# Kernel optimization log

Measured on AMD Instinct MI355X. Metric: run time of the kernel, lower is better.

## Reference

```python
import jax, jax.numpy as jnp
import numpy as np

B, T, D, H, F = 8, 1024, 512, 8, 2048
DK = D // H
EPS = 1e-3  # Keras LayerNormalization default epsilon
NEG = -1e9


def layer_norm(x, g, b):
    mu = jnp.mean(x, axis=-1, keepdims=True)
    var = jnp.mean(jnp.square(x - mu), axis=-1, keepdims=True)
    return (x - mu) * jax.lax.rsqrt(var + EPS) * g + b


def setup_inputs() -> dict:
    key = jax.random.key(0)
    ks = jax.random.split(key, 16)
    s = 1.0 / np.sqrt(D)
    sf = 1.0 / np.sqrt(F)
    x = jax.random.normal(ks[0], (B, T, D), dtype=jnp.float32)
    # binary attention mask (1 = attend). Random block-sparse-ish pattern.
    mask = (jax.random.uniform(ks[1], (B, 1, T, T)) > 0.15).astype(jnp.float32)
    return {
        "x": x,
        "mask": mask,
        "ln_in_g": jnp.ones((D,), jnp.float32),
        "ln_in_b": jnp.zeros((D,), jnp.float32),
        "Wq": jax.random.normal(ks[2], (D, D), jnp.float32) * s,
        "bq": jnp.zeros((D,), jnp.float32),
        "Wk": jax.random.normal(ks[3], (D, D), jnp.float32) * s,
        "bk": jnp.zeros((D,), jnp.float32),
        "Wv": jax.random.normal(ks[4], (D, D), jnp.float32) * s,
        "bv": jnp.zeros((D,), jnp.float32),
        "ln1_g": jnp.ones((D,), jnp.float32),
        "ln1_b": jnp.zeros((D,), jnp.float32),
        "W1": jax.random.normal(ks[5], (D, F), jnp.float32) * s,
        "b1": jnp.zeros((F,), jnp.float32),
        "W2": jax.random.normal(ks[6], (F, D), jnp.float32) * sf,
        "b2": jnp.zeros((D,), jnp.float32),
        "ln2_g": jnp.ones((D,), jnp.float32),
        "ln2_b": jnp.zeros((D,), jnp.float32),
    }


def reference(x, mask, ln_in_g, ln_in_b, Wq, bq, Wk, bk, Wv, bv,
              ln1_g, ln1_b, W1, b1, W2, b2, ln2_g, ln2_b):
    bs = x.shape[0]
    h = layer_norm(x, ln_in_g, ln_in_b)                      # [B,T,D]
    # QKV projections, split heads -> [B,H,T,DK]
    q = (h @ Wq + bq).reshape(bs, -1, H, DK).transpose(0, 2, 1, 3)
    k = (h @ Wk + bk).reshape(bs, -1, H, DK).transpose(0, 2, 1, 3)
    v = (h @ Wv + bv).reshape(bs, -1, H, DK).transpose(0, 2, 1, 3)
    scores = jnp.einsum('bhtd,bhsd->bhts', q, k) / np.sqrt(DK)
    scores = scores + NEG * (1.0 - mask)                     # additive mask
    probs = jax.nn.softmax(scores, axis=-1)                  # dropout: identity at inference
    attn = jnp.einsum('bhts,bhsd->bhtd', probs, v)
    attn = attn.transpose(0, 2, 1, 3).reshape(bs, -1, H * DK)
    # residual with ORIGINAL inputs (pre-ln_in), as in call() -> attend(inputs,...)
    attn = attn + x
    a = layer_norm(attn, ln1_g, ln1_b)
    f = jax.nn.relu(a @ W1 + b1) @ W2 + b2
    out = layer_norm(f + a, ln2_g, ln2_b)
    return out
```

## Files before the change

### kernel.cpp

```cpp
#include <hip/hip_runtime.h>

typedef unsigned short u16;
typedef unsigned long long u64;
typedef __bf16 bf16x8 __attribute__((ext_vector_type(8)));
typedef float f32x4 __attribute__((ext_vector_type(4)));

#define B_ 8
#define T_ 1024
#define D_ 512
#define H_ 8
#define DK_ 64
#define F_ 2048

__device__ __forceinline__ u16 f2bf(float f) {
    unsigned u = __float_as_uint(f);
    u += 0x7fffu + ((u >> 16) & 1u);
    return (u16)(u >> 16);
}

__device__ __forceinline__ void tile_transcvt(
    const float* __restrict__ W, u16* __restrict__ WT, int K, int N, int k0, int n0,
    u16 (*t)[72])
{
    const int tid = threadIdx.x;
    const int r = tid >> 2, c4 = (tid & 3) * 16;
    const float* src = W + (size_t)(k0 + r) * N + n0 + c4;
#pragma unroll
    for (int j = 0; j < 16; j += 4) {
        float4 v = *(const float4*)(src + j);
        t[r][c4 + j]     = f2bf(v.x);
        t[r][c4 + j + 1] = f2bf(v.y);
        t[r][c4 + j + 2] = f2bf(v.z);
        t[r][c4 + j + 3] = f2bf(v.w);
    }
    __syncthreads();
    u16 tmp[16];
#pragma unroll
    for (int j = 0; j < 16; ++j) tmp[j] = t[c4 + j][r];
    u16* dst = WT + (size_t)(n0 + r) * K + k0 + c4;
    *(uint4*)dst       = *(uint4*)&tmp[0];
    *(uint4*)(dst + 8) = *(uint4*)&tmp[8];
}

__global__ __launch_bounds__(256) void prep_all(
    const float* __restrict__ Wq, const float* __restrict__ Wk, const float* __restrict__ Wv,
    const float* __restrict__ bq, const float* __restrict__ bk, const float* __restrict__ bv,
    const float* __restrict__ W1, const float* __restrict__ W2,
    const float* __restrict__ mask,
    u16* __restrict__ WqkvT, u16* __restrict__ W1T, u16* __restrict__ W2T,
    float* __restrict__ bias, u64* __restrict__ Mb)
{
    __shared__ u16 t[64][72];
    const int blk = blockIdx.x;
    const int tid = threadIdx.x;
    if (blk < 192) {
        const int k0 = (blk & 7) * 64;
        const int n0 = (blk >> 3) * 64;
        const float* W = (n0 < 512) ? Wq : (n0 < 1024 ? Wk : Wv);
        if (k0 == 0 && tid < 64) {
            int n = n0 + tid;
            bias[n] = (n < 512) ? bq[n] : (n < 1024 ? bk[n - 512] : bv[n - 1024]);
        }
        const int r = tid >> 2, c4 = (tid & 3) * 16;
        const float* src = W + (size_t)(k0 + r) * 512 + (n0 & 511) + c4;
#pragma unroll
        for (int j = 0; j < 16; j += 4) {
            float4 v = *(const float4*)(src + j);
            t[r][c4 + j]     = f2bf(v.x);
            t[r][c4 + j + 1] = f2bf(v.y);
            t[r][c4 + j + 2] = f2bf(v.z);
            t[r][c4 + j + 3] = f2bf(v.w);
        }
        __syncthreads();
        u16 tmp[16];
#pragma unroll
        for (int j = 0; j < 16; ++j) tmp[j] = t[c4 + j][r];
        u16* dst = WqkvT + (size_t)(n0 + r) * 512 + k0 + c4;
        *(uint4*)dst       = *(uint4*)&tmp[0];
        *(uint4*)(dst + 8) = *(uint4*)&tmp[8];
    } else if (blk < 448) {
        const int idx = blk - 192;
        tile_transcvt(W1, W1T, 512, 2048, (idx & 7) * 64, (idx >> 3) * 64, t);
    } else if (blk < 704) {
        const int idx = blk - 448;
        tile_transcvt(W2, W2T, 2048, 512, (idx & 31) * 64, (idx >> 5) * 64, t);
    } else {
        const int idx = blk - 704;
        int gw = (idx * 256 + tid) >> 6;
        int lane = tid & 63;
#pragma unroll
        for (int i = 0; i < 16; ++i) {
            size_t chunk = (size_t)gw * 16 + i;
            float v = mask[chunk * 64 + lane];
            u64 bm = __ballot(v > 0.5f);
            if (lane == 0) Mb[chunk] = bm;
        }
    }
}

__global__ __launch_bounds__(256) void ln_kernel(
    const float* __restrict__ X, const float* __restrict__ R,
    const float* __restrict__ g, const float* __restrict__ bt,
    u16* __restrict__ ob, float* __restrict__ of)
{
    int wave = threadIdx.x >> 6, lane = threadIdx.x & 63;
    int row = blockIdx.x * 4 + wave;
    size_t base = (size_t)row * D_ + lane * 8;
    float v[8];
    float4 a0 = *(const float4*)(X + base);
    float4 a1 = *(const float4*)(X + base + 4);
    v[0]=a0.x; v[1]=a0.y; v[2]=a0.z; v[3]=a0.w;
    v[4]=a1.x; v[5]=a1.y; v[6]=a1.z; v[7]=a1.w;
    if (R) {
        float4 r0 = *(const float4*)(R + base);
        float4 r1 = *(const float4*)(R + base + 4);
        v[0]+=r0.x; v[1]+=r0.y; v[2]+=r0.z; v[3]+=r0.w;
        v[4]+=r1.x; v[5]+=r1.y; v[6]+=r1.z; v[7]+=r1.w;
    }
    float s = 0.f, q = 0.f;
#pragma unroll
    for (int j = 0; j < 8; ++j) { s += v[j]; q += v[j] * v[j]; }
#pragma unroll
    for (int off = 32; off > 0; off >>= 1) {
        s += __shfl_xor(s, off);
        q += __shfl_xor(q, off);
    }
    float mu = s * (1.0f / D_);
    float var = q * (1.0f / D_) - mu * mu;
    float rstd = rsqrtf(var + 1e-3f);
    int c0 = lane * 8;
    float y[8];
#pragma unroll
    for (int j = 0; j < 8; ++j) y[j] = (v[j] - mu) * rstd * g[c0 + j] + bt[c0 + j];
    if (ob) {
        u16 t[8];
#pragma unroll
        for (int j = 0; j < 8; ++j) t[j] = f2bf(y[j]);
        *(uint4*)(ob + base) = *(uint4*)t;
    }
    if (of) {
        float4 o0, o1;
        o0.x=y[0]; o0.y=y[1]; o0.z=y[2]; o0.w=y[3];
        o1.x=y[4]; o1.y=y[5]; o1.z=y[6]; o1.w=y[7];
        *(float4*)(of + base) = o0;
        *(float4*)(of + base + 4) = o1;
    }
}

template<int BN, int RELU, int OUTBF>
__global__ __launch_bounds__(256) void gemm_db(
    const u16* __restrict__ A, const u16* __restrict__ BT,
    const float* __restrict__ bias, u16* __restrict__ Cb,
    float* __restrict__ Cf, int M, int N, int K)
{
    constexpr int NI = BN / 32;
    __shared__ u16 As[2][128 * 32];
    __shared__ u16 Bs[2][BN * 32];
    const int nb = gridDim.x;
    const int flat = blockIdx.y * nb + blockIdx.x;
    const int xcd = flat & 7;
    const int idx = flat >> 3;
    const int nblk = idx >> 3;
    const int mblk = xcd * 8 + (idx & 7);
    const int tid = threadIdx.x;
    const int wave = tid >> 6, lane = tid & 63;
    const int quad = lane >> 4, l16 = lane & 15;
    const int wr = wave >> 1, wc = wave & 1;
    const int rowBase = mblk * 128;
    const int colBase = nblk * BN;
    const int lr = lane >> 2;
    const int lc = (lane & 3) * 8;
    const u16* Abase = A  + (size_t)(rowBase + lr) * K + lc;
    const u16* Bbase = BT + (size_t)(colBase + lr) * K + lc;

    auto stage = [&](int k0, int buf) {
#pragma unroll
        for (int c = 0; c < 2; ++c) {
            int chunk = wave * 2 + c;
            const u16* gp = Abase + (size_t)(chunk * 16) * K + k0;
            __builtin_amdgcn_global_load_lds(
                (const __attribute__((address_space(1))) unsigned int*)gp,
                (__attribute__((address_space(3))) unsigned int*)&As[buf][chunk * 512],
                16, 0, 0);
        }
#pragma unroll
        for (int c = 0; c < BN / 64; ++c) {
            int chunk = wave * (BN / 64) + c;
            const u16* gp = Bbase + (size_t)(chunk * 16) * K + k0;
            __builtin_amdgcn_global_load_lds(
                (const __attribute__((address_space(1))) unsigned int*)gp,
                (__attribute__((address_space(3))) unsigned int*)&Bs[buf][chunk * 512],
                16, 0, 0);
        }
    };

    f32x4 acc[4][NI] = {};
    stage(0, 0);
    for (int k0 = 0; k0 < K; k0 += 32) {
        const int buf = (k0 >> 5) & 1;
        __syncthreads();
        if (k0 + 32 < K) stage(k0 + 32, buf ^ 1);
        bf16x8 af[4], bfr[NI];
#pragma unroll
        for (int i = 0; i < 4; ++i)
            af[i] = *(const bf16x8*)&As[buf][(wr * 64 + i * 16 + l16) * 32 + quad * 8];
#pragma unroll
        for (int j = 0; j < NI; ++j)
            bfr[j] = *(const bf16x8*)&Bs[buf][(wc * (BN / 2) + j * 16 + l16) * 32 + quad * 8];
#pragma unroll
        for (int i = 0; i < 4; ++i)
#pragma unroll
            for (int j = 0; j < NI; ++j)
                acc[i][j] = __builtin_amdgcn_mfma_f32_16x16x32_bf16(af[i], bfr[j], acc[i][j], 0, 0, 0);
    }
#pragma unroll
    for (int i = 0; i < 4; ++i) {
        int row0 = rowBase + wr * 64 + i * 16 + quad * 4;
#pragma unroll
        for (int j = 0; j < NI; ++j) {
            int col = colBase + wc * (BN / 2) + j * 16 + l16;
            float bv = bias[col];
#pragma unroll
            for (int r = 0; r < 4; ++r) {
                float v = acc[i][j][r] + bv;
                if (RELU) v = fmaxf(v, 0.0f);
                if (OUTBF) Cb[(size_t)(row0 + r) * N + col] = f2bf(v);
                else       Cf[(size_t)(row0 + r) * N + col] = v;
            }
        }
    }
}

__global__ __launch_bounds__(256) void vtrans(const u16* __restrict__ QKV, u16* __restrict__ Vt)
{
    int blk = blockIdx.x;
    int bh = blk >> 4;
    int t0 = (blk & 15) * 64;
    int b = bh >> 3, h = bh & 7;
    __shared__ u16 tile[64][72];
    int tid = threadIdx.x;
    int r = tid >> 2;
    int c = (tid & 3) * 16;
    const u16* src = QKV + ((size_t)(b * T_) + t0 + r) * (3 * D_) + 2 * D_ + h * DK_ + c;
    *(uint4*)&tile[r][c]     = *(const uint4*)(src);
    *(uint4*)&tile[r][c + 8] = *(const uint4*)(src + 8);
    __syncthreads();
    u16 tmp[16];
#pragma unroll
    for (int j = 0; j < 16; ++j) tmp[j] = tile[c + j][r];
    u16* dst = Vt + ((size_t)bh * DK_ + r) * T_ + t0 + c;
    *(uint4*)dst       = *(uint4*)&tmp[0];
    *(uint4*)(dst + 8) = *(uint4*)&tmp[8];
}

#define APAD 72
__global__ __launch_bounds__(256) void attn_kernel(
    const u16* __restrict__ QKV, const u16* __restrict__ Vt,
    const u64* __restrict__ Mb, float* __restrict__ Out)
{
    const int flat = blockIdx.x + 16 * (blockIdx.y + 8 * blockIdx.z);
    const int xcd = flat & 7, slot = flat >> 3;
    const int bh = xcd * 8 + (slot >> 4);
    const int qt = slot & 15;
    const int b = bh >> 3, h = bh & 7;
    const int qBase = qt * 64;
    const int tid = threadIdx.x;
    const int wave = tid >> 6, lane = tid & 63;
    const int quad = lane >> 4, l16 = lane & 15;
    __shared__ u16 Ks[64][APAD];
    __shared__ u16 Vs[64][APAD];
    __shared__ u16 Ps[4][16][APAD];

    const int qRow = qBase + wave * 16 + l16;
    const u16* qptr = QKV + ((size_t)(b * T_) + qRow) * (3 * D_) + h * DK_;
    bf16x8 qf0 = *(const bf16x8*)(qptr + quad * 8);
    bf16x8 qf1 = *(const bf16x8*)(qptr + 32 + quad * 8);

    float l_i[4] = {0.f, 0.f, 0.f, 0.f};
    f32x4 o[4] = {{0,0,0,0},{0,0,0,0},{0,0,0,0},{0,0,0,0}};

    const int sr = tid >> 2;
    const int sc = (tid & 3) * 8;
    const u16* Kg = QKV + (size_t)(b * T_) * (3 * D_) + D_ + h * DK_;
    const u16* Vg = Vt + (size_t)(b * H_ + h) * DK_ * T_;
    const u64* Mg = Mb + ((size_t)(b * T_) + qBase + wave * 16 + quad * 4) * (T_ / 64);

    uint4 kb0 = *(const uint4*)(Kg + (size_t)sr * (3 * D_) + sc);
    uint4 kb1 = *(const uint4*)(Kg + (size_t)sr * (3 * D_) + sc + 32);
    uint4 vb0 = *(const uint4*)(Vg + (size_t)sr * T_ + sc);
    uint4 vb1 = *(const uint4*)(Vg + (size_t)sr * T_ + sc + 32);
    u64 m64[4];
#pragma unroll
    for (int r = 0; r < 4; ++r) m64[r] = Mg[(size_t)r * (T_ / 64)];

    for (int s0 = 0; s0 < T_; s0 += 64) {
        __syncthreads();
        *(uint4*)&Ks[sr][sc]      = kb0;
        *(uint4*)&Ks[sr][sc + 32] = kb1;
        *(uint4*)&Vs[sr][sc]      = vb0;
        *(uint4*)&Vs[sr][sc + 32] = vb1;
        __syncthreads();
        u64 mcur[4];
#pragma unroll
        for (int r = 0; r < 4; ++r) mcur[r] = m64[r];
        if (s0 + 64 < T_) {
            int s1 = s0 + 64;
            kb0 = *(const uint4*)(Kg + (size_t)(s1 + sr) * (3 * D_) + sc);
            kb1 = *(const uint4*)(Kg + (size_t)(s1 + sr) * (3 * D_) + sc + 32);
            vb0 = *(const uint4*)(Vg + (size_t)sr * T_ + s1 + sc);
            vb1 = *(const uint4*)(Vg + (size_t)sr * T_ + s1 + sc + 32);
#pragma unroll
            for (int r = 0; r < 4; ++r) m64[r] = Mg[(size_t)r * (T_ / 64) + (s1 >> 6)];
        }

#pragma unroll
        for (int n = 0; n < 4; ++n) {
            f32x4 s4 = {0.f, 0.f, 0.f, 0.f};
            bf16x8 kf0 = *(const bf16x8*)&Ks[n * 16 + l16][quad * 8];
            bf16x8 kf1 = *(const bf16x8*)&Ks[n * 16 + l16][32 + quad * 8];
            s4 = __builtin_amdgcn_mfma_f32_16x16x32_bf16(qf0, kf0, s4, 0, 0, 0);
            s4 = __builtin_amdgcn_mfma_f32_16x16x32_bf16(qf1, kf1, s4, 0, 0, 0);
#pragma unroll
            for (int r = 0; r < 4; ++r) {
                float p = __expf(fmaf(s4[r], 0.125f, -10.0f));
                p = ((mcur[r] >> (n * 16 + l16)) & 1ull) ? p : 0.0f;
                l_i[r] += p;
                Ps[wave][quad * 4 + r][n * 16 + l16] = f2bf(p);
            }
        }
        bf16x8 pf0 = *(const bf16x8*)&Ps[wave][l16][quad * 8];
        bf16x8 pf1 = *(const bf16x8*)&Ps[wave][l16][32 + quad * 8];
#pragma unroll
        for (int dt = 0; dt < 4; ++dt) {
            bf16x8 vf0 = *(const bf16x8*)&Vs[dt * 16 + l16][quad * 8];
            bf16x8 vf1 = *(const bf16x8*)&Vs[dt * 16 + l16][32 + quad * 8];
            o[dt] = __builtin_amdgcn_mfma_f32_16x16x32_bf16(pf0, vf0, o[dt], 0, 0, 0);
            o[dt] = __builtin_amdgcn_mfma_f32_16x16x32_bf16(pf1, vf1, o[dt], 0, 0, 0);
        }
    }
#pragma unroll
    for (int off = 1; off < 16; off <<= 1) {
#pragma unroll
        for (int r = 0; r < 4; ++r) l_i[r] += __shfl_xor(l_i[r], off);
    }
    float inv[4];
#pragma unroll
    for (int r = 0; r < 4; ++r) inv[r] = 1.0f / l_i[r];
    const int orow = qBase + wave * 16 + quad * 4;
    float* Ob = Out + ((size_t)(b * T_) + orow) * D_ + h * DK_;
#pragma unroll
    for (int dt = 0; dt < 4; ++dt) {
#pragma unroll
        for (int r = 0; r < 4; ++r)
            Ob[(size_t)r * D_ + dt * 16 + l16] = o[dt][r] * inv[r];
    }
}

extern "C" void kernel_launch(void* const* d_in, const int* in_sizes, int n_in,
                              void* d_out, int out_size, void* d_ws, size_t ws_size,
                              hipStream_t stream)
{
    const float* x       = (const float*)d_in[0];
    const float* mask    = (const float*)d_in[1];
    const float* ln_in_g = (const float*)d_in[2];
    const float* ln_in_b = (const float*)d_in[3];
    const float* Wq      = (const float*)d_in[4];
    const float* bq      = (const float*)d_in[5];
    const float* Wk      = (const float*)d_in[6];
    const float* bk      = (const float*)d_in[7];
    const float* Wv      = (const float*)d_in[8];
    const float* bv      = (const float*)d_in[9];
    const float* ln1_g   = (const float*)d_in[10];
    const float* ln1_b   = (const float*)d_in[11];
    const float* W1      = (const float*)d_in[12];
    const float* b1      = (const float*)d_in[13];
    const float* W2      = (const float*)d_in[14];
    const float* b2      = (const float*)d_in[15];
    const float* ln2_g   = (const float*)d_in[16];
    const float* ln2_b   = (const float*)d_in[17];
    float* out = (float*)d_out;

    char* ws = (char*)d_ws;
    size_t off = 0;
    auto alloc = [&](size_t bytes) -> void* {
        void* p = ws + off;
        off = (off + bytes + 255) & ~(size_t)255;
        return p;
    };
    u16*   WqkvT   = (u16*)alloc((size_t)1536 * 512 * 2);
    u16*   W1T     = (u16*)alloc((size_t)2048 * 512 * 2);
    u16*   W2T     = (u16*)alloc((size_t)512 * 2048 * 2);
    float* bias_q  = (float*)alloc(1536 * 4);
    u64*   Mb      = (u64*)alloc((size_t)B_ * T_ * (T_ / 64) * 8);
    u16*   h_bf    = (u16*)alloc((size_t)8192 * 512 * 2);
    u16*   QKV     = (u16*)alloc((size_t)8192 * 1536 * 2);
    u16*   Vt      = (u16*)alloc((size_t)B_ * H_ * DK_ * T_ * 2);
    float* attn    = (float*)alloc((size_t)8192 * 512 * 4);
    u16*   a_bf    = (u16*)alloc((size_t)8192 * 512 * 2);
    float* a_f     = (float*)alloc((size_t)8192 * 512 * 4);
    u16*   f1      = (u16*)alloc((size_t)8192 * 2048 * 2);
    float* f2      = (float*)alloc((size_t)8192 * 512 * 4);
    if (off > ws_size) return;

    prep_all<<<2752, 256, 0, stream>>>(Wq, Wk, Wv, bq, bk, bv, W1, W2, mask,
                                       WqkvT, W1T, W2T, bias_q, Mb);

    ln_kernel<<<2048, 256, 0, stream>>>(x, nullptr, ln_in_g, ln_in_b, h_bf, nullptr);

    gemm_db<128, 0, 1><<<dim3(1536 / 128, 8192 / 128), 256, 0, stream>>>(
        h_bf, WqkvT, bias_q, QKV, nullptr, 8192, 1536, 512);

    vtrans<<<1024, 256, 0, stream>>>(QKV, Vt);

    attn_kernel<<<dim3(T_ / 64, H_, B_), 256, 0, stream>>>(QKV, Vt, Mb, attn);

    ln_kernel<<<2048, 256, 0, stream>>>(attn, x, ln1_g, ln1_b, a_bf, a_f);

    gemm_db<128, 1, 1><<<dim3(2048 / 128, 8192 / 128), 256, 0, stream>>>(
        a_bf, W1T, b1, f1, nullptr, 8192, 2048, 512);

    gemm_db<64, 0, 0><<<dim3(512 / 64, 8192 / 128), 256, 0, stream>>>(
        f1, W2T, b2, nullptr, f2, 8192, 512, 2048);

    ln_kernel<<<2048, 256, 0, stream>>>(f2, a_f, ln2_g, ln2_b, nullptr, out);
}
```

Before: 291.8 us.

## Split-K FFN2 with atomics, bf16 attention output, and bias-prefilled accumulator

The FFN2 GEMM is split into two K halves accumulated with float atomicAdd into f2, which the LN1 kernel prefills with b2. This doubles the block count for the 512-wide GEMM. Attention now writes bf16 instead of fp32, and the fp32 copy of the LN1 output is dropped, so the final LN reads the bf16 residual. Mask-word loads in attention are no longer prefetched a tile ahead. The changes cut memory traffic and raise parallelism, at the cost of some precision and atomic contention.

Result: no change. 296.9 us (+1.7%).

```diff
diff --git a/kernel.cpp b/kernel.cpp
--- a/kernel.cpp
+++ b/kernel.cpp
@@ -16,6 +16,9 @@
     unsigned u = __float_as_uint(f);
     u += 0x7fffu + ((u >> 16) & 1u);
     return (u16)(u >> 16);
+}
+__device__ __forceinline__ float bf2f(u16 v) {
+    return __uint_as_float((unsigned)v << 16);
 }
 
 __device__ __forceinline__ void tile_transcvt(
@@ -98,24 +101,51 @@
     }
 }
 
-__global__ __launch_bounds__(256) void ln_kernel(
-    const float* __restrict__ X, const float* __restrict__ R,
+template<int XBF, int RBF, int OB, int OF, int FILL>
+__global__ __launch_bounds__(256) void ln_t(
+    const void* __restrict__ Xv, const void* __restrict__ Rv,
     const float* __restrict__ g, const float* __restrict__ bt,
-    u16* __restrict__ ob, float* __restrict__ of)
+    u16* __restrict__ ob, float* __restrict__ of,
+    const float* __restrict__ fillsrc, float* __restrict__ filldst)
 {
     int wave = threadIdx.x >> 6, lane = threadIdx.x & 63;
     int row = blockIdx.x * 4 + wave;
     size_t base = (size_t)row * D_ + lane * 8;
+    int c0 = lane * 8;
     float v[8];
-    float4 a0 = *(const float4*)(X + base);
-    float4 a1 = *(const float4*)(X + base + 4);
-    v[0]=a0.x; v[1]=a0.y; v[2]=a0.z; v[3]=a0.w;
-    v[4]=a1.x; v[5]=a1.y; v[6]=a1.z; v[7]=a1.w;
-    if (R) {
-        float4 r0 = *(const float4*)(R + base);
-        float4 r1 = *(const float4*)(R + base + 4);
-        v[0]+=r0.x; v[1]+=r0.y; v[2]+=r0.z; v[3]+=r0.w;
-        v[4]+=r1.x; v[5]+=r1.y; v[6]+=r1.z; v[7]+=r1.w;
+    if (XBF) {
+        const u16* X = (const u16*)Xv;
+        uint4 a = *(const uint4*)(X + base);
+        u16 tu[8]; *(uint4*)tu = a;
+#pragma unroll
+        for (int j = 0; j < 8; ++j) v[j] = bf2f(tu[j]);
+    } else {
+        const float* X = (const float*)Xv;
+        float4 a0 = *(const float4*)(X + base);
+        float4 a1 = *(const float4*)(X + base + 4);
+        v[0]=a0.x; v[1]=a0.y; v[2]=a0.z; v[3]=a0.w;
+        v[4]=a1.x; v[5]=a1.y; v[6]=a1.z; v[7]=a1.w;
+    }
+    if (Rv) {
+        if (RBF) {
+            const u16* R = (const u16*)Rv;
+            uint4 a = *(const uint4*)(R + base);
+            u16 tu[8]; *(uint4*)tu = a;
+#pragma unroll
+            for (int j = 0; j < 8; ++j) v[j] += bf2f(tu[j]);
+        } else {
+            const float* R = (const float*)Rv;
+            float4 r0 = *(const float4*)(R + base);
+            float4 r1 = *(const float4*)(R + base + 4);
+            v[0]+=r0.x; v[1]+=r0.y; v[2]+=r0.z; v[3]+=r0.w;
+            v[4]+=r1.x; v[5]+=r1.y; v[6]+=r1.z; v[7]+=r1.w;
+        }
+    }
+    if (FILL) {
+        float4 f0 = *(const float4*)(fillsrc + c0);
+        float4 f1v = *(const float4*)(fillsrc + c0 + 4);
+        *(float4*)(filldst + base) = f0;
+        *(float4*)(filldst + base + 4) = f1v;
     }
     float s = 0.f, q = 0.f;
 #pragma unroll
@@ -128,17 +158,16 @@
     float mu = s * (1.0f / D_);
     float var = q * (1.0f / D_) - mu * mu;
     float rstd = rsqrtf(var + 1e-3f);
-    int c0 = lane * 8;
     float y[8];
 #pragma unroll
     for (int j = 0; j < 8; ++j) y[j] = (v[j] - mu) * rstd * g[c0 + j] + bt[c0 + j];
-    if (ob) {
+    if (OB) {
         u16 t[8];
 #pragma unroll
         for (int j = 0; j < 8; ++j) t[j] = f2bf(y[j]);
         *(uint4*)(ob + base) = *(uint4*)t;
     }
-    if (of) {
+    if (OF) {
         float4 o0, o1;
         o0.x=y[0]; o0.y=y[1]; o0.z=y[2]; o0.w=y[3];
         o1.x=y[4]; o1.y=y[5]; o1.z=y[6]; o1.w=y[7];
@@ -147,11 +176,11 @@
     }
 }
 
-template<int BN, int RELU, int OUTBF>
+template<int BN, int RELU, int OUT>
 __global__ __launch_bounds__(256) void gemm_db(
     const u16* __restrict__ A, const u16* __restrict__ BT,
     const float* __restrict__ bias, u16* __restrict__ Cb,
-    float* __restrict__ Cf, int M, int N, int K)
+    float* __restrict__ Cf, int N, int K, int KS)
 {
     constexpr int NI = BN / 32;
     __shared__ u16 As[2][128 * 32];
@@ -170,8 +199,9 @@
     const int colBase = nblk * BN;
     const int lr = lane >> 2;
     const int lc = (lane & 3) * 8;
-    const u16* Abase = A  + (size_t)(rowBase + lr) * K + lc;
-    const u16* Bbase = BT + (size_t)(colBase + lr) * K + lc;
+    const int kOff = blockIdx.z * KS;
+    const u16* Abase = A  + (size_t)(rowBase + lr) * K + kOff + lc;
+    const u16* Bbase = BT + (size_t)(colBase + lr) * K + kOff + lc;
 
     auto stage = [&](int k0, int buf) {
 #pragma unroll
@@ -196,10 +226,10 @@
 
     f32x4 acc[4][NI] = {};
     stage(0, 0);
-    for (int k0 = 0; k0 < K; k0 += 32) {
+    for (int k0 = 0; k0 < KS; k0 += 32) {
         const int buf = (k0 >> 5) & 1;
         __syncthreads();
-        if (k0 + 32 < K) stage(k0 + 32, buf ^ 1);
+        if (k0 + 32 < KS) stage(k0 + 32, buf ^ 1);
         bf16x8 af[4], bfr[NI];
 #pragma unroll
         for (int i = 0; i < 4; ++i)
@@ -219,13 +249,14 @@
 #pragma unroll
         for (int j = 0; j < NI; ++j) {
             int col = colBase + wc * (BN / 2) + j * 16 + l16;
-            float bv = bias[col];
+            float bv = (OUT == 2) ? 0.0f : bias[col];
 #pragma unroll
             for (int r = 0; r < 4; ++r) {
                 float v = acc[i][j][r] + bv;
                 if (RELU) v = fmaxf(v, 0.0f);
-                if (OUTBF) Cb[(size_t)(row0 + r) * N + col] = f2bf(v);
-                else       Cf[(size_t)(row0 + r) * N + col] = v;
+                if (OUT == 2)      atomicAdd(&Cf[(size_t)(row0 + r) * N + col], v);
+                else if (OUT == 1) Cb[(size_t)(row0 + r) * N + col] = f2bf(v);
+                else               Cf[(size_t)(row0 + r) * N + col] = v;
             }
         }
     }
@@ -256,7 +287,7 @@
 #define APAD 72
 __global__ __launch_bounds__(256) void attn_kernel(
     const u16* __restrict__ QKV, const u16* __restrict__ Vt,
-    const u64* __restrict__ Mb, float* __restrict__ Out)
+    const u64* __restrict__ Mb, u16* __restrict__ Out)
 {
     const int flat = blockIdx.x + 16 * (blockIdx.y + 8 * blockIdx.z);
     const int xcd = flat & 7, slot = flat >> 3;
@@ -289,9 +320,6 @@
     uint4 kb1 = *(const uint4*)(Kg + (size_t)sr * (3 * D_) + sc + 32);
     uint4 vb0 = *(const uint4*)(Vg + (size_t)sr * T_ + sc);
     uint4 vb1 = *(const uint4*)(Vg + (size_t)sr * T_ + sc + 32);
-    u64 m64[4];
-#pragma unroll
-    for (int r = 0; r < 4; ++r) m64[r] = Mg[(size_t)r * (T_ / 64)];
 
     for (int s0 = 0; s0 < T_; s0 += 64) {
         __syncthreads();
@@ -300,18 +328,17 @@
         *(uint4*)&Vs[sr][sc]      = vb0;
         *(uint4*)&Vs[sr][sc + 32] = vb1;
         __syncthreads();
-        u64 mcur[4];
-#pragma unroll
-        for (int r = 0; r < 4; ++r) mcur[r] = m64[r];
         if (s0 + 64 < T_) {
             int s1 = s0 + 64;
             kb0 = *(const uint4*)(Kg + (size_t)(s1 + sr) * (3 * D_) + sc);
             kb1 = *(const uint4*)(Kg + (size_t)(s1 + sr) * (3 * D_) + sc + 32);
             vb0 = *(const uint4*)(Vg + (size_t)sr * T_ + s1 + sc);
             vb1 = *(const uint4*)(Vg + (size_t)sr * T_ + s1 + sc + 32);
-#pragma unroll
-            for (int r = 0; r < 4; ++r) m64[r] = Mg[(size_t)r * (T_ / 64) + (s1 >> 6)];
-        }
+        }
+
+        u64 m64[4];
+#pragma unroll
+        for (int r = 0; r < 4; ++r) m64[r] = Mg[(size_t)r * (T_ / 64) + (s0 >> 6)];
 
 #pragma unroll
         for (int n = 0; n < 4; ++n) {
@@ -323,7 +350,7 @@
 #pragma unroll
             for (int r = 0; r < 4; ++r) {
                 float p = __expf(fmaf(s4[r], 0.125f, -10.0f));
-                p = ((mcur[r] >> (n * 16 + l16)) & 1ull) ? p : 0.0f;
+                p = ((m64[r] >> (n * 16 + l16)) & 1ull) ? p : 0.0f;
                 l_i[r] += p;
                 Ps[wave][quad * 4 + r][n * 16 + l16] = f2bf(p);
             }
@@ -347,12 +374,12 @@
 #pragma unroll
     for (int r = 0; r < 4; ++r) inv[r] = 1.0f / l_i[r];
     const int orow = qBase + wave * 16 + quad * 4;
-    float* Ob = Out + ((size_t)(b * T_) + orow) * D_ + h * DK_;
+    u16* Ob = Out + ((size_t)(b * T_) + orow) * D_ + h * DK_;
 #pragma unroll
     for (int dt = 0; dt < 4; ++dt) {
 #pragma unroll
         for (int r = 0; r < 4; ++r)
-            Ob[(size_t)r * D_ + dt * 16 + l16] = o[dt][r] * inv[r];
+            Ob[(size_t)r * D_ + dt * 16 + l16] = f2bf(o[dt][r] * inv[r]);
     }
 }
 
@@ -395,9 +422,8 @@
     u16*   h_bf    = (u16*)alloc((size_t)8192 * 512 * 2);
     u16*   QKV     = (u16*)alloc((size_t)8192 * 1536 * 2);
     u16*   Vt      = (u16*)alloc((size_t)B_ * H_ * DK_ * T_ * 2);
-    float* attn    = (float*)alloc((size_t)8192 * 512 * 4);
+    u16*   attn_bf = (u16*)alloc((size_t)8192 * 512 * 2);
     u16*   a_bf    = (u16*)alloc((size_t)8192 * 512 * 2);
-    float* a_f     = (float*)alloc((size_t)8192 * 512 * 4);
     u16*   f1      = (u16*)alloc((size_t)8192 * 2048 * 2);
     float* f2      = (float*)alloc((size_t)8192 * 512 * 4);
     if (off > ws_size) return;
@@ -405,22 +431,25 @@
     prep_all<<<2752, 256, 0, stream>>>(Wq, Wk, Wv, bq, bk, bv, W1, W2, mask,
                                        WqkvT, W1T, W2T, bias_q, Mb);
 
-    ln_kernel<<<2048, 256, 0, stream>>>(x, nullptr, ln_in_g, ln_in_b, h_bf, nullptr);
-
-    gemm_db<128, 0, 1><<<dim3(1536 / 128, 8192 / 128), 256, 0, stream>>>(
-        h_bf, WqkvT, bias_q, QKV, nullptr, 8192, 1536, 512);
+    ln_t<0, 0, 1, 0, 0><<<2048, 256, 0, stream>>>(
+        x, nullptr, ln_in_g, ln_in_b, h_bf, nullptr, nullptr, nullptr);
+
+    gemm_db<128, 0, 1><<<dim3(12, 64, 1), 256, 0, stream>>>(
+        h_bf, WqkvT, bias_q, QKV, nullptr, 1536, 512, 512);
 
     vtrans<<<1024, 256, 0, stream>>>(QKV, Vt);
 
-    attn_kernel<<<dim3(T_ / 64, H_, B_), 256, 0, stream>>>(QKV, Vt, Mb, attn);
-
-    ln_kernel<<<2048, 256, 0, stream>>>(attn, x, ln1_g, ln1_b, a_bf, a_f);
-
-    gemm_db<128, 1, 1><<<dim3(2048 / 128, 8192 / 128), 256, 0, stream>>>(
-        a_bf, W1T, b1, f1, nullptr, 8192, 2048, 512);
-
-    gemm_db<64, 0, 0><<<dim3(512 / 64, 8192 / 128), 256, 0, stream>>>(
-        f1, W2T, b2, nullptr, f2, 8192, 512, 2048);
-
-    ln_kernel<<<2048, 256, 0, stream>>>(f2, a_f, ln2_g, ln2_b, nullptr, out);
-}
+    attn_kernel<<<dim3(16, 8, 8), 256, 0, stream>>>(QKV, Vt, Mb, attn_bf);
+
+    ln_t<1, 0, 1, 0, 1><<<2048, 256, 0, stream>>>(
+        attn_bf, x, ln1_g, ln1_b, a_bf, nullptr, b2, f2);
+
+    gemm_db<128, 1, 1><<<dim3(16, 64, 1), 256, 0, stream>>>(
+        a_bf, W1T, b1, f1, nullptr, 2048, 512, 512);
+
+    gemm_db<64, 0, 2><<<dim3(8, 64, 2), 256, 0, stream>>>(
+        f1, W2T, nullptr, nullptr, f2, 512, 2048, 1024);
+
+    ln_t<0, 1, 0, 1, 0><<<2048, 256, 0, stream>>>(
+        f2, a_bf, ln2_g, ln2_b, nullptr, out, nullptr, nullptr);
+}
```
